# Kernel optimization log

Hardware: AMD Instinct MI355X
Metric: run time of the kernel (lower is better)

## Reference

```python
import jax, jax.numpy as jnp
import numpy as np

EPS = 1e-8


def setup_inputs() -> dict:
    key = jax.random.key(0)
    k1, k2 = jax.random.split(key)
    N, F, K, C = 16384, 64, 32, 100
    membership = jax.random.uniform(k1, (N, F, K), dtype=jnp.float32)
    teacher_probs = jax.random.uniform(k2, (N, C), dtype=jnp.float32)
    return {"membership": membership, "teacher_probs": teacher_probs}


def reference(membership, teacher_probs):
    # membership: [N, F, K]  soft bin assignments per feature
    # teacher_probs: [N, C]  teacher class distribution per sample
    N, F, K = membership.shape
    bin_mass = membership.sum(axis=0) + EPS  # [F, K]
    # Contraction form of (membership[:, :, :, None] * teacher_probs[:, None, None, :]).sum(0)
    # avoids the N*F*K*C intermediate.
    centroids = jnp.einsum('nfk,nc->fkc', membership, teacher_probs) / bin_mass[:, :, None]  # [F, K, C]
    # Intra-bin: minimize entropy of each bin's class distribution, mass-weighted.
    intra_entropy = -jnp.sum(centroids * jnp.log(centroids + EPS), axis=2)  # [F, K]
    loss_intra = jnp.sum(intra_entropy * bin_mass) / N
    # Inter-bin: maximize entropy of the mixture of adjacent bins
    # (loss_inter is negative entropy summed, added with +0.5 weight).
    mixture = 0.5 * (centroids[:, :-1, :] + centroids[:, 1:, :])  # [F, K-1, C]
    loss_inter = jnp.sum(mixture * jnp.log(mixture + EPS))
    return loss_intra + 0.5 * loss_inter
```

## Files before the change

### kernel.cpp

```cpp
#include <hip/hip_runtime.h>
#include <hip/hip_bf16.h>

#define NS   16384
#define FKD  2048
#define CD   100
#define CP   112
#define NKC  32
#define PHASES 16
#define EPSF 1e-8f
#define SFK  (FKD * CP)
#define NGRP (NS / 8)

typedef float f32x4 __attribute__((ext_vector_type(4)));
typedef short bf16x8 __attribute__((ext_vector_type(8)));

__device__ inline unsigned short f2bf(float f) {
    unsigned int u = __float_as_uint(f);
    u += 0x7FFFu + ((u >> 16) & 1u);
    return (unsigned short)(u >> 16);
}

__device__ __forceinline__ void gload16(const float* g, const float* l) {
    __builtin_amdgcn_global_load_lds(
        (const __attribute__((address_space(1))) void*)g,
        (__attribute__((address_space(3))) void*)l, 16, 0, 0);
}

__global__ __launch_bounds__(256) void ebl_prep(
    const float* __restrict__ tp, unsigned short* __restrict__ Bp)
{
    const int idx = blockIdx.x * 256 + threadIdx.x;
    if (idx >= NGRP * CP) return;
    const int g = idx / CP, c = idx - g * CP;
    unsigned short v[8];
    if (c < CD) {
        const float* p = tp + (size_t)g * 8 * CD + c;
        #pragma unroll
        for (int j = 0; j < 8; ++j) v[j] = f2bf(p[(size_t)j * CD]);
    } else {
        const unsigned short fill = (c == CD) ? 0x3F80 : 0;
        #pragma unroll
        for (int j = 0; j < 8; ++j) v[j] = fill;
    }
    *reinterpret_cast<uint4*>(Bp + (size_t)idx * 8) = *reinterpret_cast<const uint4*>(v);
}

__global__ __launch_bounds__(128) void ebl_gemm(
    const float* __restrict__ mem, const unsigned short* __restrict__ Bp,
    unsigned short* __restrict__ spart)
{
    __shared__ float At[3 * 2 * 2048];

    const int t  = threadIdx.x;
    const int w  = t >> 6;
    const int l  = t & 63;
    const int lg = l >> 4, lr = l & 15;
    const int m0 = blockIdx.x * 128;
    const int kc = blockIdx.y;
    const int n0 = kc * (PHASES * 32);
    const int gb = n0 >> 3;

    const float* gbase = mem + (size_t)(n0 + lg) * FKD + (m0 + w * 64 + lr * 4);

    f32x4 acc[4][7];
    #pragma unroll
    for (int i = 0; i < 4; ++i)
        #pragma unroll
        for (int nt = 0; nt < 7; ++nt) acc[i][nt] = (f32x4){0.f, 0.f, 0.f, 0.f};

    bf16x8 b0[7], b1[7];
    int o0 = (0 * 2 + w) * 2048, o1 = (1 * 2 + w) * 2048, o2 = (2 * 2 + w) * 2048;

#define SB() __builtin_amdgcn_sched_barrier(0)
#define STAGE(bo, p) { \
    const float* gs = gbase + (size_t)(p) * 32 * FKD; \
    _Pragma("unroll") \
    for (int q = 0; q < 8; ++q) \
        gload16(gs + (size_t)q * 4 * FKD, At + (bo) + q * 256); \
    SB(); }
#define LOADB(dst, p) { \
    const unsigned short* bq = Bp + ((size_t)(gb + (p) * 4 + lg) * CP + lr) * 8; \
    _Pragma("unroll") \
    for (int nt = 0; nt < 7; ++nt) dst[nt] = *reinterpret_cast<const bf16x8*>(bq + nt * 128); \
    SB(); }
#define WAITV(n) { asm volatile("s_waitcnt vmcnt(" #n ")" ::: "memory"); SB(); }
#define COMPUTE(bo, bB) { \
    bf16x8 af[4]; \
    _Pragma("unroll") \
    for (int i = 0; i < 4; ++i) \
        _Pragma("unroll") \
        for (int j = 0; j < 8; ++j) { \
            float v = At[(bo) + (2 * lg + (j >> 2)) * 256 + (j & 3) * 64 + i * 16 + lr]; \
            af[i][j] = (short)f2bf(v); } \
    _Pragma("unroll") \
    for (int i = 0; i < 4; ++i) \
        _Pragma("unroll") \
        for (int nt = 0; nt < 7; ++nt) \
            acc[i][nt] = __builtin_amdgcn_mfma_f32_16x16x32_bf16(af[i], bB[nt], acc[i][nt], 0, 0, 0); }

    STAGE(o0, 0)
    LOADB(b0, 0)
    STAGE(o1, 1)

    for (int ph = 0; ph < PHASES - 2; ph += 2) {
        LOADB(b1, ph + 1)
        STAGE(o2, ph + 2)
        WAITV(23)
        COMPUTE(o0, b0)
        LOADB(b0, ph + 2)
        STAGE(o0, ph + 3)
        WAITV(23)
        COMPUTE(o1, b1)
        const int tmp = o2; o2 = o1; o1 = o0; o0 = tmp;
    }
    LOADB(b1, PHASES - 1)
    WAITV(15)
    COMPUTE(o0, b0)
    WAITV(0)
    COMPUTE(o1, b1)

#undef SB
#undef STAGE
#undef LOADB
#undef WAITV
#undef COMPUTE

    unsigned short* sp = spart + (size_t)kc * SFK;
    #pragma unroll
    for (int i = 0; i < 4; ++i) {
        #pragma unroll
        for (int nt = 0; nt < 7; ++nt) {
            const int c = nt * 16 + lr;
            #pragma unroll
            for (int r = 0; r < 4; ++r) {
                const int mm = m0 + w * 64 + i * 16 + lg * 4 + r;
                sp[(size_t)mm * CP + c] = f2bf(acc[i][nt][r]);
            }
        }
    }
}

__global__ __launch_bounds__(256) void ebl_reduce(
    const unsigned short* __restrict__ spart, float* __restrict__ S)
{
    const int idx = blockIdx.x * 256 + threadIdx.x;
    if (idx >= SFK / 2) return;
    float s0 = 0.f, s1 = 0.f;
    for (int p = 0; p < NKC; ++p) {
        const unsigned raw = *reinterpret_cast<const unsigned*>(spart + (size_t)p * SFK + (size_t)idx * 2);
        s0 += __uint_as_float(raw << 16);
        s1 += __uint_as_float(raw & 0xFFFF0000u);
    }
    *reinterpret_cast<float2*>(S + (size_t)idx * 2) = make_float2(s0, s1);
}

__global__ __launch_bounds__(256) void ebl_entropy(
    const float* __restrict__ S, float* __restrict__ fpart)
{
    __shared__ float Ss[32 * CP];
    __shared__ float massL[32];
    __shared__ float red[4];
    const int t = threadIdx.x;
    const int f = blockIdx.x;

    for (int idx = t; idx < 32 * CP; idx += 256)
        Ss[idx] = S[(size_t)f * 32 * CP + idx];
    __syncthreads();
    if (t < 32) massL[t] = Ss[t * CP + CD] + EPSF;
    __syncthreads();

    float a_int = 0.f, a_mix = 0.f;
    for (int idx = t; idx < 32 * CD; idx += 256) {
        const int k = idx / CD, c = idx - k * CD;
        const float cent = Ss[k * CP + c] / massL[k];
        a_int -= cent * logf(cent + EPSF) * massL[k];
    }
    for (int idx = t; idx < 31 * CD; idx += 256) {
        const int k = idx / CD, c = idx - k * CD;
        const float mix = 0.5f * (Ss[k * CP + c] / massL[k] + Ss[(k + 1) * CP + c] / massL[k + 1]);
        a_mix += mix * logf(mix + EPSF);
    }

    float part = a_int * (1.0f / (float)NS) + 0.5f * a_mix;
    #pragma unroll
    for (int off = 32; off > 0; off >>= 1) part += __shfl_down(part, off);
    if ((t & 63) == 0) red[t >> 6] = part;
    __syncthreads();
    if (t == 0) fpart[f] = (red[0] + red[1]) + (red[2] + red[3]);
}

__global__ void ebl_finalize(const float* __restrict__ fpart, float* __restrict__ out) {
    float v = fpart[threadIdx.x];
    #pragma unroll
    for (int off = 32; off > 0; off >>= 1) v += __shfl_down(v, off);
    if (threadIdx.x == 0) out[0] = v;
}

extern "C" void kernel_launch(void* const* d_in, const int* in_sizes, int n_in,
                              void* d_out, int out_size, void* d_ws, size_t ws_size,
                              hipStream_t stream)
{
    const float* mem = (const float*)d_in[0];
    const float* tp  = (const float*)d_in[1];
    float* out = (float*)d_out;

    const size_t bpBytes = (size_t)NGRP * CP * 8 * 2;

    unsigned short* Bp    = (unsigned short*)d_ws;
    unsigned short* spart = (unsigned short*)((char*)d_ws + bpBytes);
    float*          S     = (float*)((char*)spart + (size_t)NKC * SFK * 2);
    float*          fpart = S + SFK;

    ebl_prep<<<(NGRP * CP + 255) / 256, 256, 0, stream>>>(tp, Bp);
    dim3 grid(FKD / 128, NKC);
    ebl_gemm<<<grid, 128, 0, stream>>>(mem, Bp, spart);
    ebl_reduce<<<(SFK / 2 + 255) / 256, 256, 0, stream>>>(spart, S);
    ebl_entropy<<<64, 256, 0, stream>>>(S, fpart);
    ebl_finalize<<<1, 64, 0, stream>>>(fpart, out);
}
```

Baseline: 51.48 us.

## Share LDS A tile across four waves with barrier-synced double buffering

Result: slower. 63.70 us (+23.7%).

```diff
diff --git a/kernel.cpp b/kernel.cpp
--- a/kernel.cpp
+++ b/kernel.cpp
@@ -13,6 +13,7 @@
 
 typedef float f32x4 __attribute__((ext_vector_type(4)));
 typedef short bf16x8 __attribute__((ext_vector_type(8)));
+typedef unsigned uint4v __attribute__((ext_vector_type(4)));
 
 __device__ inline unsigned short f2bf(float f) {
     unsigned int u = __float_as_uint(f);
@@ -45,23 +46,21 @@
     *reinterpret_cast<uint4*>(Bp + (size_t)idx * 8) = *reinterpret_cast<const uint4*>(v);
 }
 
-__global__ __launch_bounds__(128) void ebl_gemm(
+__global__ __launch_bounds__(256) void ebl_gemm(
     const float* __restrict__ mem, const unsigned short* __restrict__ Bp,
     unsigned short* __restrict__ spart)
 {
-    __shared__ float At[3 * 2 * 2048];
+    __shared__ float At[2 * 32 * 256];
 
     const int t  = threadIdx.x;
     const int w  = t >> 6;
     const int l  = t & 63;
     const int lg = l >> 4, lr = l & 15;
-    const int m0 = blockIdx.x * 128;
+    const int m0 = blockIdx.x * 256;
     const int kc = blockIdx.y;
     const int n0 = kc * (PHASES * 32);
     const int gb = n0 >> 3;
 
-    const float* gbase = mem + (size_t)(n0 + lg) * FKD + (m0 + w * 64 + lr * 4);
-
     f32x4 acc[4][7];
     #pragma unroll
     for (int i = 0; i < 4; ++i)
@@ -69,61 +68,86 @@
         for (int nt = 0; nt < 7; ++nt) acc[i][nt] = (f32x4){0.f, 0.f, 0.f, 0.f};
 
     bf16x8 b0[7], b1[7];
-    int o0 = (0 * 2 + w) * 2048, o1 = (1 * 2 + w) * 2048, o2 = (2 * 2 + w) * 2048;
+    const int o0 = 0, o1 = 32 * 256;
 
 #define SB() __builtin_amdgcn_sched_barrier(0)
-#define STAGE(bo, p) { \
-    const float* gs = gbase + (size_t)(p) * 32 * FKD; \
-    _Pragma("unroll") \
-    for (int q = 0; q < 8; ++q) \
-        gload16(gs + (size_t)q * 4 * FKD, At + (bo) + q * 256); \
+#define BAR() { SB(); __builtin_amdgcn_s_barrier(); SB(); }
+#define STAGE(o, s) { \
+    _Pragma("unroll") \
+    for (int q = 0; q < 8; ++q) { \
+        const int rr = w * 8 + q; \
+        gload16(mem + (size_t)(n0 + (s) * 32 + rr) * FKD + m0 + l * 4, \
+                At + (o) + rr * 256); } \
     SB(); }
-#define LOADB(dst, p) { \
-    const unsigned short* bq = Bp + ((size_t)(gb + (p) * 4 + lg) * CP + lr) * 8; \
+#define LOADB(dst, s) { \
+    const unsigned short* bq = Bp + ((size_t)(gb + (s) * 4 + lg) * CP + lr) * 8; \
     _Pragma("unroll") \
     for (int nt = 0; nt < 7; ++nt) dst[nt] = *reinterpret_cast<const bf16x8*>(bq + nt * 128); \
     SB(); }
 #define WAITV(n) { asm volatile("s_waitcnt vmcnt(" #n ")" ::: "memory"); SB(); }
-#define COMPUTE(bo, bB) { \
-    bf16x8 af[4]; \
-    _Pragma("unroll") \
-    for (int i = 0; i < 4; ++i) \
+#define READCVT(o, AF) \
+    bf16x8 AF[4]; \
+    { \
+    _Pragma("unroll") \
+    for (int i = 0; i < 4; ++i) { \
+        uint4v u; \
         _Pragma("unroll") \
-        for (int j = 0; j < 8; ++j) { \
-            float v = At[(bo) + (2 * lg + (j >> 2)) * 256 + (j & 3) * 64 + i * 16 + lr]; \
-            af[i][j] = (short)f2bf(v); } \
+        for (int jj = 0; jj < 4; ++jj) { \
+            float f0 = At[(o) + (8 * lg + 2 * jj)     * 256 + w * 64 + i * 16 + lr]; \
+            float f1 = At[(o) + (8 * lg + 2 * jj + 1) * 256 + w * 64 + i * 16 + lr]; \
+            unsigned uu; \
+            asm("v_cvt_pk_bf16_f32 %0, %1, %2" : "=v"(uu) : "v"(f0), "v"(f1)); \
+            u[jj] = uu; \
+        } \
+        AF[i] = __builtin_bit_cast(bf16x8, u); \
+    } \
+    SB(); }
+#define MFMAS(AF, bB) { \
     _Pragma("unroll") \
     for (int i = 0; i < 4; ++i) \
         _Pragma("unroll") \
         for (int nt = 0; nt < 7; ++nt) \
-            acc[i][nt] = __builtin_amdgcn_mfma_f32_16x16x32_bf16(af[i], bB[nt], acc[i][nt], 0, 0, 0); }
+            acc[i][nt] = __builtin_amdgcn_mfma_f32_16x16x32_bf16(AF[i], bB[nt], acc[i][nt], 0, 0, 0); }
 
     STAGE(o0, 0)
     LOADB(b0, 0)
-    STAGE(o1, 1)
-
-    for (int ph = 0; ph < PHASES - 2; ph += 2) {
-        LOADB(b1, ph + 1)
-        STAGE(o2, ph + 2)
-        WAITV(23)
-        COMPUTE(o0, b0)
-        LOADB(b0, ph + 2)
-        STAGE(o0, ph + 3)
-        WAITV(23)
-        COMPUTE(o1, b1)
-        const int tmp = o2; o2 = o1; o1 = o0; o0 = tmp;
+
+    for (int s = 0; s < PHASES - 2; s += 2) {
+        LOADB(b1, s + 1)
+        STAGE(o1, s + 1)
+        WAITV(15)
+        BAR()
+        READCVT(o0, afA)
+        BAR()
+        MFMAS(afA, b0)
+        LOADB(b0, s + 2)
+        STAGE(o0, s + 2)
+        WAITV(15)
+        BAR()
+        READCVT(o1, afB)
+        BAR()
+        MFMAS(afB, b1)
     }
     LOADB(b1, PHASES - 1)
+    STAGE(o1, PHASES - 1)
     WAITV(15)
-    COMPUTE(o0, b0)
+    BAR()
+    READCVT(o0, afC)
+    BAR()
+    MFMAS(afC, b0)
     WAITV(0)
-    COMPUTE(o1, b1)
+    BAR()
+    READCVT(o1, afD)
+    BAR()
+    MFMAS(afD, b1)
 
 #undef SB
+#undef BAR
 #undef STAGE
 #undef LOADB
 #undef WAITV
-#undef COMPUTE
+#undef READCVT
+#undef MFMAS
 
     unsigned short* sp = spart + (size_t)kc * SFK;
     #pragma unroll
@@ -212,8 +236,8 @@
     float*          fpart = S + SFK;
 
     ebl_prep<<<(NGRP * CP + 255) / 256, 256, 0, stream>>>(tp, Bp);
-    dim3 grid(FKD / 128, NKC);
-    ebl_gemm<<<grid, 128, 0, stream>>>(mem, Bp, spart);
+    dim3 grid(FKD / 256, NKC);
+    ebl_gemm<<<grid, 256, 0, stream>>>(mem, Bp, spart);
     ebl_reduce<<<(SFK / 2 + 255) / 256, 256, 0, stream>>>(spart, S);
     ebl_entropy<<<64, 256, 0, stream>>>(S, fpart);
     ebl_finalize<<<1, 64, 0, stream>>>(fpart, out);
```

## Fuse split-K reduction, entropy, and finalize into one tail kernel

Applied to the files above, without the earlier changes.

Result: no change. 51.92 us (+0.8%).

```diff
diff --git a/kernel.cpp b/kernel.cpp
--- a/kernel.cpp
+++ b/kernel.cpp
@@ -27,9 +27,11 @@
 }
 
 __global__ __launch_bounds__(256) void ebl_prep(
-    const float* __restrict__ tp, unsigned short* __restrict__ Bp)
+    const float* __restrict__ tp, unsigned short* __restrict__ Bp,
+    unsigned* __restrict__ cnt)
 {
     const int idx = blockIdx.x * 256 + threadIdx.x;
+    if (idx == 0) *cnt = 0;
     if (idx >= NGRP * CP) return;
     const int g = idx / CP, c = idx - g * CP;
     unsigned short v[8];
@@ -140,31 +142,31 @@
     }
 }
 
-__global__ __launch_bounds__(256) void ebl_reduce(
-    const unsigned short* __restrict__ spart, float* __restrict__ S)
-{
-    const int idx = blockIdx.x * 256 + threadIdx.x;
-    if (idx >= SFK / 2) return;
-    float s0 = 0.f, s1 = 0.f;
-    for (int p = 0; p < NKC; ++p) {
-        const unsigned raw = *reinterpret_cast<const unsigned*>(spart + (size_t)p * SFK + (size_t)idx * 2);
-        s0 += __uint_as_float(raw << 16);
-        s1 += __uint_as_float(raw & 0xFFFF0000u);
-    }
-    *reinterpret_cast<float2*>(S + (size_t)idx * 2) = make_float2(s0, s1);
-}
-
-__global__ __launch_bounds__(256) void ebl_entropy(
-    const float* __restrict__ S, float* __restrict__ fpart)
+__global__ __launch_bounds__(256) void ebl_tail(
+    const unsigned short* __restrict__ spart, float* __restrict__ fpart,
+    unsigned* __restrict__ cnt, float* __restrict__ out)
 {
     __shared__ float Ss[32 * CP];
     __shared__ float massL[32];
     __shared__ float red[4];
+    __shared__ int lastFlag;
     const int t = threadIdx.x;
     const int f = blockIdx.x;
-
-    for (int idx = t; idx < 32 * CP; idx += 256)
-        Ss[idx] = S[(size_t)f * 32 * CP + idx];
+    const size_t base = (size_t)f * 32 * CP;
+
+    for (int v = t; v < 32 * CP / 8; v += 256) {
+        float s[8];
+        #pragma unroll
+        for (int j = 0; j < 8; ++j) s[j] = 0.f;
+        for (int p = 0; p < NKC; ++p) {
+            uint4 raw = *reinterpret_cast<const uint4*>(spart + (size_t)p * SFK + base + (size_t)v * 8);
+            const unsigned short* u = reinterpret_cast<const unsigned short*>(&raw);
+            #pragma unroll
+            for (int j = 0; j < 8; ++j) s[j] += __uint_as_float((unsigned)u[j] << 16);
+        }
+        #pragma unroll
+        for (int j = 0; j < 8; ++j) Ss[v * 8 + j] = s[j];
+    }
     __syncthreads();
     if (t < 32) massL[t] = Ss[t * CP + CD] + EPSF;
     __syncthreads();
@@ -186,14 +188,22 @@
     for (int off = 32; off > 0; off >>= 1) part += __shfl_down(part, off);
     if ((t & 63) == 0) red[t >> 6] = part;
     __syncthreads();
-    if (t == 0) fpart[f] = (red[0] + red[1]) + (red[2] + red[3]);
-}
-
-__global__ void ebl_finalize(const float* __restrict__ fpart, float* __restrict__ out) {
-    float v = fpart[threadIdx.x];
-    #pragma unroll
-    for (int off = 32; off > 0; off >>= 1) v += __shfl_down(v, off);
-    if (threadIdx.x == 0) out[0] = v;
+
+    if (t == 0) {
+        fpart[f] = (red[0] + red[1]) + (red[2] + red[3]);
+        __threadfence();
+        const unsigned ticket =
+            __hip_atomic_fetch_add(cnt, 1u, __ATOMIC_ACQ_REL, __HIP_MEMORY_SCOPE_AGENT);
+        lastFlag = (ticket == 63);
+    }
+    __syncthreads();
+
+    if (lastFlag && t < 64) {
+        float v = __hip_atomic_load(&fpart[t], __ATOMIC_ACQUIRE, __HIP_MEMORY_SCOPE_AGENT);
+        #pragma unroll
+        for (int off = 32; off > 0; off >>= 1) v += __shfl_down(v, off);
+        if (t == 0) out[0] = v;
+    }
 }
 
 extern "C" void kernel_launch(void* const* d_in, const int* in_sizes, int n_in,
@@ -208,13 +218,11 @@
 
     unsigned short* Bp    = (unsigned short*)d_ws;
     unsigned short* spart = (unsigned short*)((char*)d_ws + bpBytes);
-    float*          S     = (float*)((char*)spart + (size_t)NKC * SFK * 2);
-    float*          fpart = S + SFK;
-
-    ebl_prep<<<(NGRP * CP + 255) / 256, 256, 0, stream>>>(tp, Bp);
+    float*          fpart = (float*)((char*)spart + (size_t)NKC * SFK * 2);
+    unsigned*       cnt   = (unsigned*)(fpart + 64);
+
+    ebl_prep<<<(NGRP * CP + 255) / 256, 256, 0, stream>>>(tp, Bp, cnt);
     dim3 grid(FKD / 128, NKC);
     ebl_gemm<<<grid, 128, 0, stream>>>(mem, Bp, spart);
-    ebl_reduce<<<(SFK / 2 + 255) / 256, 256, 0, stream>>>(spart, S);
-    ebl_entropy<<<64, 256, 0, stream>>>(S, fpart);
-    ebl_finalize<<<1, 64, 0, stream>>>(fpart, out);
-}
+    ebl_tail<<<64, 256, 0, stream>>>(spart, fpart, cnt, out);
+}
```
